# Kernel tuning notes

Measured on AMD Instinct MI355X. Metric: run time of the kernel, lower is better.

The kernel has to match this reference:

```python
import jax, jax.numpy as jnp
import numpy as np

B, C, H, W = 2, 512, 64, 64
NUM_GROUPS = 32
EPS = 1e-6


def setup_inputs() -> dict:
    key = jax.random.key(0)
    ks = jax.random.split(key, 6)
    s = 1.0 / np.sqrt(C)
    return {
        "x": jax.random.normal(ks[0], (B, C, H, W), dtype=jnp.float32),
        "gn_scale": jnp.ones((C,), jnp.float32),
        "gn_bias": jnp.zeros((C,), jnp.float32),
        "wq": jax.random.normal(ks[1], (C, C), jnp.float32) * s,
        "bq": jnp.zeros((C,), jnp.float32),
        "wk": jax.random.normal(ks[2], (C, C), jnp.float32) * s,
        "bk": jnp.zeros((C,), jnp.float32),
        "wv": jax.random.normal(ks[3], (C, C), jnp.float32) * s,
        "bv": jnp.zeros((C,), jnp.float32),
        "wp": jax.random.normal(ks[4], (C, C), jnp.float32) * s,
        "bp": jnp.zeros((C,), jnp.float32),
    }


def group_norm(x, scale, bias):
    # x: [b, c, h, w]; GroupNorm with NUM_GROUPS groups, eps=1e-6, affine
    b, c, h, w = x.shape
    xg = x.reshape(b, NUM_GROUPS, c // NUM_GROUPS, h, w)
    mean = jnp.mean(xg, axis=(2, 3, 4), keepdims=True)
    var = jnp.var(xg, axis=(2, 3, 4), keepdims=True)
    xg = (xg - mean) * jax.lax.rsqrt(var + EPS)
    xn = xg.reshape(b, c, h, w)
    return xn * scale[None, :, None, None] + bias[None, :, None, None]


def reference(x, gn_scale, gn_bias, wq, bq, wk, bk, wv, bv, wp, bp):
    b, c, h, w = x.shape
    n = h * w
    hn = group_norm(x, gn_scale, gn_bias).reshape(b, c, n)  # [b,c,n]
    # 1x1 convs == per-pixel linear over channels
    q = jnp.einsum('dc,bcn->bdn', wq, hn) + bq[None, :, None]
    k = jnp.einsum('dc,bcn->bdn', wk, hn) + bk[None, :, None]
    v = jnp.einsum('dc,bcn->bdn', wv, hn) + bv[None, :, None]
    # attn[b,i,j] = softmax_j( q[:, :, i] . k[:, :, j] / sqrt(c) )
    attn = jnp.einsum('bci,bcj->bij', q, k) * (float(c) ** -0.5)
    attn = jax.nn.softmax(attn, axis=-1)
    out = jnp.einsum('bcj,bij->bci', v, attn)  # [b,c,n]
    out = jnp.einsum('dc,bcn->bdn', wp, out) + bp[None, :, None]
    return x + out.reshape(b, c, h, w)
```

## Files before the change

kernel.cpp:

```cpp
#include <hip/hip_runtime.h>

typedef __bf16 bf16x8 __attribute__((ext_vector_type(8)));
typedef float f32x4 __attribute__((ext_vector_type(4)));
typedef int i32x8 __attribute__((ext_vector_type(8)));


#if defined(__has_builtin)
#if __has_builtin(__builtin_amdgcn_global_load_lds)
#define HAS_GLL 1
#endif
#endif

__device__ __forceinline__ void async_copy16(const void* g, void* l) {
#ifdef HAS_GLL
    __builtin_amdgcn_global_load_lds(
        (const __attribute__((address_space(1))) unsigned int*)g,
        (__attribute__((address_space(3))) unsigned int*)l, 16, 0, 0);
#else
    *(int4*)l = *(const int4*)g;
#endif
}

__device__ __forceinline__ unsigned char to_fp8(float v) {
    return (unsigned char)(__builtin_amdgcn_cvt_pk_fp8_f32(v, v, 0, false) & 0xFF);
}

#define MXSCALE 0x7F7F7F7F

__global__ __launch_bounds__(256) void prep_kernel(
    const float* __restrict__ x, float* __restrict__ ps,
    const float* __restrict__ wq, const float* __restrict__ wk,
    const float* __restrict__ wv, const float* __restrict__ wp,
    const float* __restrict__ bq, const float* __restrict__ bk,
    unsigned char* __restrict__ wqk8, unsigned char* __restrict__ wv8,
    __bf16* __restrict__ wp_b, float* __restrict__ bqk) {
    if (blockIdx.x >= 1024) {
        int idx = (blockIdx.x - 1024) * 256 + threadIdx.x;
        wqk8[idx] = to_fp8(wq[idx]);
        wqk8[262144 + idx] = to_fp8(wk[idx]);
        wv8[idx] = to_fp8(wv[idx]);
        wp_b[idx] = (__bf16)wp[idx];
        if (idx < 512) {
            bqk[idx] = bq[idx];
            bqk[512 + idx] = bk[idx];
        }
        return;
    }
    int blk = blockIdx.x;
    const float4* base = (const float4*)x + (size_t)blk * 1024;
    float s1 = 0.f, s2 = 0.f;
#pragma unroll
    for (int i = 0; i < 4; ++i) {
        float4 v = base[threadIdx.x + (i << 8)];
        s1 += v.x + v.y + v.z + v.w;
        s2 += v.x * v.x + v.y * v.y + v.z * v.z + v.w * v.w;
    }
    for (int off = 32; off >= 1; off >>= 1) {
        s1 += __shfl_xor(s1, off);
        s2 += __shfl_xor(s2, off);
    }
    __shared__ float r1[4], r2[4];
    int wave = threadIdx.x >> 6, lane = threadIdx.x & 63;
    if (lane == 0) { r1[wave] = s1; r2[wave] = s2; }
    __syncthreads();
    if (threadIdx.x == 0) {
        ps[blk] = r1[0] + r1[1] + r1[2] + r1[3];
        ps[1024 + blk] = r2[0] + r2[1] + r2[2] + r2[3];
    }
}

__global__ __launch_bounds__(256) void gn_apply_kernel(const float* __restrict__ x,
                                                       const float* __restrict__ gn_scale,
                                                       const float* __restrict__ gn_bias,
                                                       const float* __restrict__ ps,
                                                       unsigned char* __restrict__ hn8) {
    __shared__ float tile[32][33];
    int b = blockIdx.z;
    int n0 = blockIdx.x * 32, c0 = blockIdx.y * 32;
    int tx = threadIdx.x & 31, ty = threadIdx.x >> 5;
    const float* xb = x + (size_t)b * 512 * 4096;
#pragma unroll
    for (int r = 0; r < 4; ++r) {
        int c = ty + r * 8;
        tile[c][tx] = xb[(size_t)(c0 + c) * 4096 + n0 + tx];
    }
    int c = c0 + tx;
    int g = (b << 5) + (c >> 4);
    float s1 = 0.f, s2 = 0.f;
#pragma unroll
    for (int i = 0; i < 16; ++i) {
        s1 += ps[(g << 4) + i];
        s2 += ps[1024 + (g << 4) + i];
    }
    float m = s1 * (1.f / 65536.f);
    float var = s2 * (1.f / 65536.f) - m * m;
    float rs = rsqrtf(var + 1e-6f);
    float sc = gn_scale[c] * rs;
    float bi = gn_bias[c] - m * sc;
    __syncthreads();
    unsigned char* outp = hn8 + (size_t)b * 4096 * 512;
#pragma unroll
    for (int r = 0; r < 4; ++r) {
        int n = ty + r * 8;
        float v = tile[tx][n];
        outp[(size_t)(n0 + n) * 512 + c] = to_fp8(v * sc + bi);
    }
}

template <int BN, int OUT_MODE, int BIAS_MODE>
__device__ __forceinline__ void mx_gemm_body(
    const unsigned char* __restrict__ Ab, int lda,
    const unsigned char* __restrict__ Bb, int ldb,
    void* __restrict__ C, int ldc,
    const float* __restrict__ bias, int K, float scale,
    long m0, long n0, unsigned char* As, unsigned char* Bs) {
    constexpr int NT = BN / 32;
    const int tid = threadIdx.x;
    const int lane = tid & 63, wave = tid >> 6;
    const int ln = lane & 15, q = lane >> 4;
    const int wm = (wave >> 1) << 6;
    const int wn = (wave & 1) * (BN / 2);

    f32x4 acc[4][NT] = {};

    for (int k0 = 0; k0 < K; k0 += 128) {
        __syncthreads();
#pragma unroll
        for (int p = 0; p < 4; ++p) {
            int c = (p << 8) + tid;
            int row = c >> 3, sg = ((c & 7) ^ (row & 7)) << 4;
            async_copy16(Ab + (long)row * lda + k0 + sg, &As[c << 4]);
        }
#pragma unroll
        for (int p = 0; p < BN / 32; ++p) {
            int c = (p << 8) + tid;
            int row = c >> 3, sg = ((c & 7) ^ (row & 7)) << 4;
            async_copy16(Bb + (long)row * ldb + k0 + sg, &Bs[c << 4]);
        }
        __syncthreads();
        i32x8 af[4], bf[NT];
#pragma unroll
        for (int t = 0; t < 4; ++t) {
            int row = wm + t * 16 + ln, e = row & 7;
            const unsigned char* bp = &As[row << 7];
            *(int4*)&af[t] = *(const int4*)(bp + ((((q << 1)) ^ e) << 4));
            *((int4*)&af[t] + 1) = *(const int4*)(bp + ((((q << 1) | 1) ^ e) << 4));
        }
#pragma unroll
        for (int t = 0; t < NT; ++t) {
            int row = wn + t * 16 + ln, e = row & 7;
            const unsigned char* bp = &Bs[row << 7];
            *(int4*)&bf[t] = *(const int4*)(bp + ((((q << 1)) ^ e) << 4));
            *((int4*)&bf[t] + 1) = *(const int4*)(bp + ((((q << 1) | 1) ^ e) << 4));
        }
#pragma unroll
        for (int mt = 0; mt < 4; ++mt)
#pragma unroll
            for (int nt = 0; nt < NT; ++nt)
                acc[mt][nt] = __builtin_amdgcn_mfma_scale_f32_16x16x128_f8f6f4(
                    af[mt], bf[nt], acc[mt][nt], 0, 0, 0, MXSCALE, 0, MXSCALE);
    }

#pragma unroll
    for (int mt = 0; mt < 4; ++mt) {
#pragma unroll
        for (int nt = 0; nt < NT; ++nt) {
            long col = n0 + wn + nt * 16 + ln;
#pragma unroll
            for (int r = 0; r < 4; ++r) {
                long row = m0 + wm + mt * 16 + (q << 2) + r;
                float v = acc[mt][nt][r] * scale;
                if (BIAS_MODE == 1) v += bias[row];
                if (BIAS_MODE == 2) v += bias[col];
                long off = row * (long)ldc + col;
                if (OUT_MODE == 0) {
                    ((unsigned char*)C)[off] = to_fp8(v);
                } else {
                    ((_Float16*)C)[off] = (_Float16)v;
                }
            }
        }
    }
}

__global__ __launch_bounds__(256) void qkv_kernel(
    const unsigned char* __restrict__ hn8, const unsigned char* __restrict__ wqk8,
    const unsigned char* __restrict__ wv8, const float* __restrict__ bqk,
    const float* __restrict__ bv, unsigned char* __restrict__ qk8,
    unsigned char* __restrict__ v8) {
    __shared__ __align__(16) unsigned char As[128 * 128];
    __shared__ __align__(16) unsigned char Bs[128 * 128];
    int z = blockIdx.z;
    if (z < 2) {
        long b = z;
        long m0 = (long)blockIdx.y * 128, n0 = (long)blockIdx.x * 128;
        mx_gemm_body<128, 0, 2>(hn8 + b * 4096 * 512 + m0 * 512, 512,
                                wqk8 + n0 * 512, 512,
                                qk8 + b * 4096 * 1024, 1024,
                                bqk, 512, 1.f, m0, n0, As, Bs);
    } else {
        long b = z - 2;
        int flat = blockIdx.y * 8 + blockIdx.x;
        long m0 = (long)(flat >> 6) * 128, n0 = (long)(flat & 63) * 64;
        mx_gemm_body<64, 0, 1>(wv8 + m0 * 512, 512,
                               hn8 + b * 4096 * 512 + n0 * 512, 512,
                               v8 + b * 512 * 4096, 4096,
                               bv, 512, 1.f, m0, n0, As, Bs);
    }
}

__global__ __launch_bounds__(256) void mx_s_kernel(const unsigned char* __restrict__ QK,
                                                   unsigned char* __restrict__ S,
                                                   float scale) {
    __shared__ __align__(16) unsigned char As[128 * 128];
    __shared__ __align__(16) unsigned char Bs[128 * 128];
    long b = blockIdx.z;
    long m0 = (long)blockIdx.y * 128, n0 = (long)blockIdx.x * 128;
    mx_gemm_body<128, 0, 0>(QK + b * 4096 * 1024 + m0 * 1024, 1024,
                            QK + b * 4096 * 1024 + n0 * 1024 + 512, 1024,
                            S + b * 4096 * 4096, 4096,
                            nullptr, 512, scale, m0, n0, As, Bs);
}

#define CVT4(dst, base, word)                                   \
    dst[base + 0] = __builtin_amdgcn_cvt_f32_fp8(word, 0);      \
    dst[base + 1] = __builtin_amdgcn_cvt_f32_fp8(word, 1);      \
    dst[base + 2] = __builtin_amdgcn_cvt_f32_fp8(word, 2);      \
    dst[base + 3] = __builtin_amdgcn_cvt_f32_fp8(word, 3);

__global__ __launch_bounds__(256) void softmax_kernel(unsigned char* __restrict__ S) {
    long row = blockIdx.x;
    unsigned char* srow = S + (row << 12);
    int tid = threadIdx.x;
    int4 d = ((const int4*)srow)[tid];
    float v[16];
    CVT4(v, 0, d.x)
    CVT4(v, 4, d.y)
    CVT4(v, 8, d.z)
    CVT4(v, 12, d.w)
    float mx = -1e30f;
#pragma unroll
    for (int p = 0; p < 16; ++p) mx = fmaxf(mx, v[p]);
    for (int off = 32; off >= 1; off >>= 1) mx = fmaxf(mx, __shfl_xor(mx, off));
    __shared__ float red[4], red2[4];
    int wave = tid >> 6, lane = tid & 63;
    if (lane == 0) red[wave] = mx;
    __syncthreads();
    mx = fmaxf(fmaxf(red[0], red[1]), fmaxf(red[2], red[3]));
    float s = 0.f;
#pragma unroll
    for (int p = 0; p < 16; ++p) {
        v[p] = __expf(v[p] - mx);
        s += v[p];
    }
    for (int off = 32; off >= 1; off >>= 1) s += __shfl_xor(s, off);
    if (lane == 0) red2[wave] = s;
    __syncthreads();
    s = red2[0] + red2[1] + red2[2] + red2[3];
    float inv64 = 64.f / s;
    int w[4];
#pragma unroll
    for (int i = 0; i < 4; ++i) {
        w[i] = __builtin_amdgcn_cvt_pk_fp8_f32(v[4 * i] * inv64, v[4 * i + 1] * inv64, 0, false);
        w[i] = __builtin_amdgcn_cvt_pk_fp8_f32(v[4 * i + 2] * inv64, v[4 * i + 3] * inv64, w[i], true);
    }
    ((int4*)srow)[tid] = make_int4(w[0], w[1], w[2], w[3]);
}

__global__ __launch_bounds__(256) void mx_pv_kernel(const unsigned char* __restrict__ P,
                                                    const unsigned char* __restrict__ V,
                                                    __bf16* __restrict__ O) {
    __shared__ __align__(16) unsigned char As[128 * 128];
    __shared__ __align__(16) unsigned char Bs[64 * 128];
    const int tid = threadIdx.x;
    const int lane = tid & 63, wave = tid >> 6;
    const int ln = lane & 15, q = lane >> 4;
    const int wm = (wave >> 1) << 6, wn = (wave & 1) << 5;
    const int b = blockIdx.x >> 5;
    const long m0 = (long)(blockIdx.x & 31) * 128;
    const long n0 = (long)blockIdx.y * 64;
    const unsigned char* Pb = P + ((long)b * 4096 + m0) * 4096;
    const unsigned char* Vb = V + ((long)b * 512 + n0) * 4096;

    f32x4 acc[4][2] = {};

    for (int k0 = 0; k0 < 4096; k0 += 128) {
        __syncthreads();
#pragma unroll
        for (int p = 0; p < 4; ++p) {
            int c = (p << 8) + tid;
            int row = c >> 3, sg = ((c & 7) ^ (row & 7)) << 4;
            async_copy16(Pb + (long)row * 4096 + k0 + sg, &As[c << 4]);
        }
#pragma unroll
        for (int p = 0; p < 2; ++p) {
            int c = (p << 8) + tid;
            int row = c >> 3, sg = ((c & 7) ^ (row & 7)) << 4;
            async_copy16(Vb + (long)row * 4096 + k0 + sg, &Bs[c << 4]);
        }
        __syncthreads();
        i32x8 af[4], bf[2];
#pragma unroll
        for (int t = 0; t < 4; ++t) {
            int row = wm + t * 16 + ln, e = row & 7;
            const unsigned char* ap = &As[row << 7];
            *(int4*)&af[t] = *(const int4*)(ap + ((((q << 1)) ^ e) << 4));
            *((int4*)&af[t] + 1) = *(const int4*)(ap + ((((q << 1) | 1) ^ e) << 4));
        }
#pragma unroll
        for (int t = 0; t < 2; ++t) {
            int row = wn + t * 16 + ln, e = row & 7;
            const unsigned char* bp = &Bs[row << 7];
            *(int4*)&bf[t] = *(const int4*)(bp + ((((q << 1)) ^ e) << 4));
            *((int4*)&bf[t] + 1) = *(const int4*)(bp + ((((q << 1) | 1) ^ e) << 4));
        }
#pragma unroll
        for (int mt = 0; mt < 4; ++mt)
#pragma unroll
            for (int nt = 0; nt < 2; ++nt)
                acc[mt][nt] = __builtin_amdgcn_mfma_scale_f32_16x16x128_f8f6f4(
                    af[mt], bf[nt], acc[mt][nt], 0, 0, 0, MXSCALE, 0, MXSCALE);
    }

    __bf16* Ob = O + (long)b * 4096 * 512;
#pragma unroll
    for (int mt = 0; mt < 4; ++mt) {
#pragma unroll
        for (int nt = 0; nt < 2; ++nt) {
            long col = n0 + wn + nt * 16 + ln;
#pragma unroll
            for (int r = 0; r < 4; ++r) {
                long row = m0 + wm + mt * 16 + (q << 2) + r;
                Ob[row * 512 + col] = (__bf16)(acc[mt][nt][r] * 0.015625f);
            }
        }
    }
}

__global__ __launch_bounds__(256) void proj_kernel(
    const __bf16* __restrict__ A, const __bf16* __restrict__ Bt, long bsB,
    float* __restrict__ C, long bsC, const float* __restrict__ bias,
    const float* __restrict__ resid) {
    __shared__ __align__(16) __bf16 As[128][64];
    __shared__ __align__(16) __bf16 Bs[64][64];
    const int tid = threadIdx.x;
    const int wave = tid >> 6, lane = tid & 63;
    const int q = lane >> 4, ln = lane & 15;
    const int wm = wave << 5;
    const long m0 = (long)blockIdx.y * 128, n0 = (long)blockIdx.x * 64;
    const int b = blockIdx.z;
    const __bf16* Ab = A + m0 * 512;
    const __bf16* Bb = Bt + (long)b * bsB + n0 * 512;

    f32x4 acc[2][4] = {};

    for (int k0 = 0; k0 < 512; k0 += 64) {
        __syncthreads();
#pragma unroll
        for (int p = 0; p < 4; ++p) {
            int c = (p << 8) + tid;
            int row = c >> 3, sg = (c & 7) << 3;
            async_copy16(Ab + (long)row * 512 + k0 + sg, &As[0][0] + (c << 3));
        }
#pragma unroll
        for (int p = 0; p < 2; ++p) {
            int c = (p << 8) + tid;
            int row = c >> 3, sg = (c & 7) << 3;
            async_copy16(Bb + (long)row * 512 + k0 + sg, &Bs[0][0] + (c << 3));
        }
        __syncthreads();
#pragma unroll
        for (int kk = 0; kk < 2; ++kk) {
            bf16x8 af[2], bfr[4];
#pragma unroll
            for (int mt = 0; mt < 2; ++mt)
                af[mt] = *(const bf16x8*)(&As[wm + mt * 16 + ln][(kk << 5) + (q << 3)]);
#pragma unroll
            for (int nt = 0; nt < 4; ++nt)
                bfr[nt] = *(const bf16x8*)(&Bs[nt * 16 + ln][(kk << 5) + (q << 3)]);
#pragma unroll
            for (int mt = 0; mt < 2; ++mt)
#pragma unroll
                for (int nt = 0; nt < 4; ++nt)
                    acc[mt][nt] = __builtin_amdgcn_mfma_f32_16x16x32_bf16(
                        af[mt], bfr[nt], acc[mt][nt], 0, 0, 0);
        }
    }

#pragma unroll
    for (int mt = 0; mt < 2; ++mt) {
#pragma unroll
        for (int nt = 0; nt < 4; ++nt) {
            long col = n0 + nt * 16 + ln;
#pragma unroll
            for (int r = 0; r < 4; ++r) {
                long row = m0 + wm + mt * 16 + (q << 2) + r;
                long off = (long)b * bsC + row * 4096 + col;
                C[off] = acc[mt][nt][r] + bias[row] + resid[off];
            }
        }
    }
}

extern "C" void kernel_launch(void* const* d_in, const int* in_sizes, int n_in,
                              void* d_out, int out_size, void* d_ws, size_t ws_size,
                              hipStream_t stream) {
    const float* x = (const float*)d_in[0];
    const float* gn_scale = (const float*)d_in[1];
    const float* gn_bias = (const float*)d_in[2];
    const float* wq = (const float*)d_in[3];
    const float* bq = (const float*)d_in[4];
    const float* wk = (const float*)d_in[5];
    const float* bk = (const float*)d_in[6];
    const float* wv = (const float*)d_in[7];
    const float* bv = (const float*)d_in[8];
    const float* wp = (const float*)d_in[9];
    const float* bp = (const float*)d_in[10];
    float* out = (float*)d_out;

    char* ws = (char*)d_ws;
    unsigned char* wqk8 = (unsigned char*)(ws + 0x0);
    unsigned char* wv8 = (unsigned char*)(ws + 0x80000);
    __bf16* wp_b = (__bf16*)(ws + 0xC0000);
    float* bqk = (float*)(ws + 0x140000);
    float* psum = (float*)(ws + 0x142000);
    unsigned char* hn8 = (unsigned char*)(ws + 0x150000);
    unsigned char* qk8 = (unsigned char*)(ws + 0x550000);
    unsigned char* v8 = (unsigned char*)(ws + 0xD50000);
    __bf16* o_t = (__bf16*)(ws + 0x1150000);
    unsigned char* S8 = (unsigned char*)(ws + 0x1950000);
    (void)ws_size;

    prep_kernel<<<2048, 256, 0, stream>>>(x, psum, wq, wk, wv, wp, bq, bk,
                                          wqk8, wv8, wp_b, bqk);
    gn_apply_kernel<<<dim3(128, 16, 2), 256, 0, stream>>>(x, gn_scale, gn_bias,
                                                          psum, hn8);

    qkv_kernel<<<dim3(8, 32, 4), 256, 0, stream>>>(hn8, wqk8, wv8, bqk, bv,
                                                   qk8, v8);

    const float attn_scale = 0.044194173824159216f;
    mx_s_kernel<<<dim3(32, 32, 2), 256, 0, stream>>>(qk8, S8, attn_scale);
    softmax_kernel<<<8192, 256, 0, stream>>>(S8);
    mx_pv_kernel<<<dim3(64, 8), 256, 0, stream>>>(S8, v8, o_t);

    proj_kernel<<<dim3(64, 4, 2), 256, 0, stream>>>(
        wp_b, o_t, 4096l * 512, out, 512l * 4096, bp, x);
}
```

Baseline: 188.0 us.

## Fuse softmax exp into score GEMM epilogue and double-buffer PV loads

Drops the separate softmax kernel. The score GEMM epilogue now writes exp(score)*0.25 straight to fp8 and accumulates row sums with atomics into a buffer that the prep kernel zeroes. The PV kernel divides by the row sum in its epilogue and double-buffers its LDS tiles so the next tile loads while the current one is multiplied. This removes a full read and write of the fp8 score matrix plus one kernel launch. In exchange it drops the max subtraction, which relies on scores staying small enough not to saturate fp8 or overflow exp, and it adds atomic contention.

```diff
diff --git a/kernel.cpp b/kernel.cpp
--- a/kernel.cpp
+++ b/kernel.cpp
@@ -33,7 +33,8 @@
     const float* __restrict__ wv, const float* __restrict__ wp,
     const float* __restrict__ bq, const float* __restrict__ bk,
     unsigned char* __restrict__ wqk8, unsigned char* __restrict__ wv8,
-    __bf16* __restrict__ wp_b, float* __restrict__ bqk) {
+    __bf16* __restrict__ wp_b, float* __restrict__ bqk,
+    float* __restrict__ rowsum) {
     if (blockIdx.x >= 1024) {
         int idx = (blockIdx.x - 1024) * 256 + threadIdx.x;
         wqk8[idx] = to_fp8(wq[idx]);
@@ -44,6 +45,7 @@
             bqk[idx] = bq[idx];
             bqk[512 + idx] = bk[idx];
         }
+        if (idx < 8192) rowsum[idx] = 0.f;
         return;
     }
     int blk = blockIdx.x;
@@ -112,8 +114,8 @@
     const unsigned char* __restrict__ Ab, int lda,
     const unsigned char* __restrict__ Bb, int ldb,
     void* __restrict__ C, int ldc,
-    const float* __restrict__ bias, int K, float scale,
-    long m0, long n0, unsigned char* As, unsigned char* Bs) {
+    const float* __restrict__ bias, float* __restrict__ rowsum,
+    int K, float scale, long m0, long n0, unsigned char* As, unsigned char* Bs) {
     constexpr int NT = BN / 32;
     const int tid = threadIdx.x;
     const int lane = tid & 63, wave = tid >> 6;
@@ -161,6 +163,29 @@
                     af[mt], bf[nt], acc[mt][nt], 0, 0, 0, MXSCALE, 0, MXSCALE);
     }
 
+    if (OUT_MODE == 2) {
+#pragma unroll
+        for (int mt = 0; mt < 4; ++mt) {
+#pragma unroll
+            for (int r = 0; r < 4; ++r) {
+                long row = m0 + wm + mt * 16 + (q << 2) + r;
+                float partial = 0.f;
+#pragma unroll
+                for (int nt = 0; nt < NT; ++nt) {
+                    long col = n0 + wn + nt * 16 + ln;
+                    float e = __expf(acc[mt][nt][r] * scale) * 0.25f;
+                    partial += e;
+                    ((unsigned char*)C)[row * (long)ldc + col] = to_fp8(e);
+                }
+                partial += __shfl_xor(partial, 1);
+                partial += __shfl_xor(partial, 2);
+                partial += __shfl_xor(partial, 4);
+                partial += __shfl_xor(partial, 8);
+                if (ln == 0) atomicAdd(&rowsum[row], partial);
+            }
+        }
+        return;
+    }
 #pragma unroll
     for (int mt = 0; mt < 4; ++mt) {
 #pragma unroll
@@ -172,12 +197,7 @@
                 float v = acc[mt][nt][r] * scale;
                 if (BIAS_MODE == 1) v += bias[row];
                 if (BIAS_MODE == 2) v += bias[col];
-                long off = row * (long)ldc + col;
-                if (OUT_MODE == 0) {
-                    ((unsigned char*)C)[off] = to_fp8(v);
-                } else {
-                    ((_Float16*)C)[off] = (_Float16)v;
-                }
+                ((unsigned char*)C)[row * (long)ldc + col] = to_fp8(v);
             }
         }
     }
@@ -197,7 +217,7 @@
         mx_gemm_body<128, 0, 2>(hn8 + b * 4096 * 512 + m0 * 512, 512,
                                 wqk8 + n0 * 512, 512,
                                 qk8 + b * 4096 * 1024, 1024,
-                                bqk, 512, 1.f, m0, n0, As, Bs);
+                                bqk, nullptr, 512, 1.f, m0, n0, As, Bs);
     } else {
         long b = z - 2;
         int flat = blockIdx.y * 8 + blockIdx.x;
@@ -205,73 +225,30 @@
         mx_gemm_body<64, 0, 1>(wv8 + m0 * 512, 512,
                                hn8 + b * 4096 * 512 + n0 * 512, 512,
                                v8 + b * 512 * 4096, 4096,
-                               bv, 512, 1.f, m0, n0, As, Bs);
+                               bv, nullptr, 512, 1.f, m0, n0, As, Bs);
     }
 }
 
 __global__ __launch_bounds__(256) void mx_s_kernel(const unsigned char* __restrict__ QK,
                                                    unsigned char* __restrict__ S,
+                                                   float* __restrict__ rowsum,
                                                    float scale) {
     __shared__ __align__(16) unsigned char As[128 * 128];
     __shared__ __align__(16) unsigned char Bs[128 * 128];
     long b = blockIdx.z;
     long m0 = (long)blockIdx.y * 128, n0 = (long)blockIdx.x * 128;
-    mx_gemm_body<128, 0, 0>(QK + b * 4096 * 1024 + m0 * 1024, 1024,
+    mx_gemm_body<128, 2, 0>(QK + b * 4096 * 1024 + m0 * 1024, 1024,
                             QK + b * 4096 * 1024 + n0 * 1024 + 512, 1024,
                             S + b * 4096 * 4096, 4096,
-                            nullptr, 512, scale, m0, n0, As, Bs);
-}
-
-#define CVT4(dst, base, word)                                   \
-    dst[base + 0] = __builtin_amdgcn_cvt_f32_fp8(word, 0);      \
-    dst[base + 1] = __builtin_amdgcn_cvt_f32_fp8(word, 1);      \
-    dst[base + 2] = __builtin_amdgcn_cvt_f32_fp8(word, 2);      \
-    dst[base + 3] = __builtin_amdgcn_cvt_f32_fp8(word, 3);
-
-__global__ __launch_bounds__(256) void softmax_kernel(unsigned char* __restrict__ S) {
-    long row = blockIdx.x;
-    unsigned char* srow = S + (row << 12);
-    int tid = threadIdx.x;
-    int4 d = ((const int4*)srow)[tid];
-    float v[16];
-    CVT4(v, 0, d.x)
-    CVT4(v, 4, d.y)
-    CVT4(v, 8, d.z)
-    CVT4(v, 12, d.w)
-    float mx = -1e30f;
-#pragma unroll
-    for (int p = 0; p < 16; ++p) mx = fmaxf(mx, v[p]);
-    for (int off = 32; off >= 1; off >>= 1) mx = fmaxf(mx, __shfl_xor(mx, off));
-    __shared__ float red[4], red2[4];
-    int wave = tid >> 6, lane = tid & 63;
-    if (lane == 0) red[wave] = mx;
-    __syncthreads();
-    mx = fmaxf(fmaxf(red[0], red[1]), fmaxf(red[2], red[3]));
-    float s = 0.f;
-#pragma unroll
-    for (int p = 0; p < 16; ++p) {
-        v[p] = __expf(v[p] - mx);
-        s += v[p];
-    }
-    for (int off = 32; off >= 1; off >>= 1) s += __shfl_xor(s, off);
-    if (lane == 0) red2[wave] = s;
-    __syncthreads();
-    s = red2[0] + red2[1] + red2[2] + red2[3];
-    float inv64 = 64.f / s;
-    int w[4];
-#pragma unroll
-    for (int i = 0; i < 4; ++i) {
-        w[i] = __builtin_amdgcn_cvt_pk_fp8_f32(v[4 * i] * inv64, v[4 * i + 1] * inv64, 0, false);
-        w[i] = __builtin_amdgcn_cvt_pk_fp8_f32(v[4 * i + 2] * inv64, v[4 * i + 3] * inv64, w[i], true);
-    }
-    ((int4*)srow)[tid] = make_int4(w[0], w[1], w[2], w[3]);
+                            nullptr, rowsum + b * 4096, 512, scale, m0, n0, As, Bs);
 }
 
 __global__ __launch_bounds__(256) void mx_pv_kernel(const unsigned char* __restrict__ P,
                                                     const unsigned char* __restrict__ V,
+                                                    const float* __restrict__ rowsum,
                                                     __bf16* __restrict__ O) {
-    __shared__ __align__(16) unsigned char As[128 * 128];
-    __shared__ __align__(16) unsigned char Bs[64 * 128];
+    __shared__ __align__(16) unsigned char As[2][128 * 128];
+    __shared__ __align__(16) unsigned char Bs[2][64 * 128];
     const int tid = threadIdx.x;
     const int lane = tid & 63, wave = tid >> 6;
     const int ln = lane & 15, q = lane >> 4;
@@ -284,33 +261,39 @@
 
     f32x4 acc[4][2] = {};
 
-    for (int k0 = 0; k0 < 4096; k0 += 128) {
+    auto stage = [&](unsigned char* Ad, unsigned char* Bd, int k0) {
+#pragma unroll
+        for (int p = 0; p < 4; ++p) {
+            int c = (p << 8) + tid;
+            int row = c >> 3, sg = ((c & 7) ^ (row & 7)) << 4;
+            async_copy16(Pb + (long)row * 4096 + k0 + sg, Ad + (c << 4));
+        }
+#pragma unroll
+        for (int p = 0; p < 2; ++p) {
+            int c = (p << 8) + tid;
+            int row = c >> 3, sg = ((c & 7) ^ (row & 7)) << 4;
+            async_copy16(Vb + (long)row * 4096 + k0 + sg, Bd + (c << 4));
+        }
+    };
+
+    stage(As[0], Bs[0], 0);
+    for (int it = 0; it < 32; ++it) {
+        const unsigned char* Ac = As[it & 1];
+        const unsigned char* Bc = Bs[it & 1];
         __syncthreads();
-#pragma unroll
-        for (int p = 0; p < 4; ++p) {
-            int c = (p << 8) + tid;
-            int row = c >> 3, sg = ((c & 7) ^ (row & 7)) << 4;
-            async_copy16(Pb + (long)row * 4096 + k0 + sg, &As[c << 4]);
-        }
-#pragma unroll
-        for (int p = 0; p < 2; ++p) {
-            int c = (p << 8) + tid;
-            int row = c >> 3, sg = ((c & 7) ^ (row & 7)) << 4;
-            async_copy16(Vb + (long)row * 4096 + k0 + sg, &Bs[c << 4]);
-        }
-        __syncthreads();
+        if (it < 31) stage(As[(it + 1) & 1], Bs[(it + 1) & 1], (it + 1) << 7);
         i32x8 af[4], bf[2];
 #pragma unroll
         for (int t = 0; t < 4; ++t) {
             int row = wm + t * 16 + ln, e = row & 7;
-            const unsigned char* ap = &As[row << 7];
+            const unsigned char* ap = &Ac[row << 7];
             *(int4*)&af[t] = *(const int4*)(ap + ((((q << 1)) ^ e) << 4));
             *((int4*)&af[t] + 1) = *(const int4*)(ap + ((((q << 1) | 1) ^ e) << 4));
         }
 #pragma unroll
         for (int t = 0; t < 2; ++t) {
             int row = wn + t * 16 + ln, e = row & 7;
-            const unsigned char* bp = &Bs[row << 7];
+            const unsigned char* bp = &Bc[row << 7];
             *(int4*)&bf[t] = *(const int4*)(bp + ((((q << 1)) ^ e) << 4));
             *((int4*)&bf[t] + 1) = *(const int4*)(bp + ((((q << 1) | 1) ^ e) << 4));
         }
@@ -322,16 +305,18 @@
                     af[mt], bf[nt], acc[mt][nt], 0, 0, 0, MXSCALE, 0, MXSCALE);
     }
 
+    const float* rsb = rowsum + (long)b * 4096;
     __bf16* Ob = O + (long)b * 4096 * 512;
 #pragma unroll
     for (int mt = 0; mt < 4; ++mt) {
 #pragma unroll
-        for (int nt = 0; nt < 2; ++nt) {
-            long col = n0 + wn + nt * 16 + ln;
-#pragma unroll
-            for (int r = 0; r < 4; ++r) {
-                long row = m0 + wm + mt * 16 + (q << 2) + r;
-                Ob[row * 512 + col] = (__bf16)(acc[mt][nt][r] * 0.015625f);
+        for (int r = 0; r < 4; ++r) {
+            long row = m0 + wm + mt * 16 + (q << 2) + r;
+            float inv = 1.f / rsb[row];
+#pragma unroll
+            for (int nt = 0; nt < 2; ++nt) {
+                long col = n0 + wn + nt * 16 + ln;
+                Ob[row * 512 + col] = (__bf16)(acc[mt][nt][r] * inv);
             }
         }
     }
@@ -424,6 +409,7 @@
     __bf16* wp_b = (__bf16*)(ws + 0xC0000);
     float* bqk = (float*)(ws + 0x140000);
     float* psum = (float*)(ws + 0x142000);
+    float* rowsum = (float*)(ws + 0x144000);
     unsigned char* hn8 = (unsigned char*)(ws + 0x150000);
     unsigned char* qk8 = (unsigned char*)(ws + 0x550000);
     unsigned char* v8 = (unsigned char*)(ws + 0xD50000);
@@ -432,7 +418,7 @@
     (void)ws_size;
 
     prep_kernel<<<2048, 256, 0, stream>>>(x, psum, wq, wk, wv, wp, bq, bk,
-                                          wqk8, wv8, wp_b, bqk);
+                                          wqk8, wv8, wp_b, bqk, rowsum);
     gn_apply_kernel<<<dim3(128, 16, 2), 256, 0, stream>>>(x, gn_scale, gn_bias,
                                                           psum, hn8);
 
@@ -440,9 +426,8 @@
                                                    qk8, v8);
 
     const float attn_scale = 0.044194173824159216f;
-    mx_s_kernel<<<dim3(32, 32, 2), 256, 0, stream>>>(qk8, S8, attn_scale);
-    softmax_kernel<<<8192, 256, 0, stream>>>(S8);
-    mx_pv_kernel<<<dim3(64, 8), 256, 0, stream>>>(S8, v8, o_t);
+    mx_s_kernel<<<dim3(32, 32, 2), 256, 0, stream>>>(qk8, S8, rowsum, attn_scale);
+    mx_pv_kernel<<<dim3(64, 8), 256, 0, stream>>>(S8, v8, rowsum, o_t);
 
     proj_kernel<<<dim3(64, 4, 2), 256, 0, stream>>>(
         wp_b, o_t, 4096l * 512, out, 512l * 4096, bp, x);
```

Measured after the change: 220.4 us. 17.2% more time.
